# Performance work log

Measured on AMD Instinct MI355X. Metric: run time of the kernel, lower is better.

The kernel has to match this reference:

```python
import jax, jax.numpy as jnp
import numpy as np

ODE_UNFOLDS = 6
MOTOR_SIZE = 3
EPS = 1e-8

def _conv(x, w, b, stride):
    y = jax.lax.conv_general_dilated(x, w, (stride, stride), 'VALID',
                                     dimension_numbers=('NCHW', 'OIHW', 'NCHW'))
    return jax.nn.relu(y + b[None, :, None, None])

def _conv_head(x, w1, b1, w2, b2, w3, b3, w4, b4, w5, b5, fc_w, fc_b):
    # x: [B, T, 3, 66, 200] -> features [B, T, 128]
    B, T = x.shape[0], x.shape[1]
    h = x.reshape(B * T, *x.shape[2:])
    h = _conv(h, w1, b1, 2)  # [BT,24,31,98]
    h = _conv(h, w2, b2, 2)  # [BT,36,14,47]
    h = _conv(h, w3, b3, 2)  # [BT,48,5,22]
    h = _conv(h, w4, b4, 1)  # [BT,64,3,20]
    h = _conv(h, w5, b5, 1)  # [BT,64,1,18]
    h = h.reshape(B * T, -1)
    h = jax.nn.relu(h @ fc_w + fc_b)
    return h.reshape(B, T, -1)

def _ltc_step(inputs, v, s_mu, s_sigma, s_w, s_erev, mu, sigma, w, erev, gleak, vleak, cm):
    # inputs: [B,S], v: [B,N]
    # sensory synapse activations (constant over the ODE unfolds)
    s_act = s_w * jax.nn.sigmoid((inputs[:, :, None] - s_mu) * s_sigma)  # [B,S,N]
    w_num_s = jnp.sum(s_act * s_erev, axis=1)  # [B,N]
    w_den_s = jnp.sum(s_act, axis=1)           # [B,N]
    cm_t = cm * ODE_UNFOLDS  # cm / (elapsed=1 / ode_unfolds)
    for _ in range(ODE_UNFOLDS):
        w_act = w * jax.nn.sigmoid((v[:, :, None] - mu) * sigma)  # [B,N,N]
        w_num = jnp.sum(w_act * erev, axis=1) + w_num_s
        w_den = jnp.sum(w_act, axis=1) + w_den_s
        v = (cm_t * v + gleak * vleak + w_num) / (cm_t + gleak + w_den + EPS)
    return v[:, :MOTOR_SIZE], v

def reference(x, w1, b1, w2, b2, w3, b3, w4, b4, w5, b5, fc_w, fc_b,
              s_mu, s_sigma, s_w, s_erev, mu, sigma, w, erev, gleak, vleak, cm):
    y = _conv_head(x, w1, b1, w2, b2, w3, b3, w4, b4, w5, b5, fc_w, fc_b)  # [B,T,128]
    B, T, _ = y.shape
    N = mu.shape[0]
    v0 = jnp.zeros((B, N), dtype=y.dtype)

    def step(v, inp):
        out, v = _ltc_step(inp, v, s_mu, s_sigma, s_w, s_erev, mu, sigma, w, erev, gleak, vleak, cm)
        return v, out

    _, outs = jax.lax.scan(step, v0, jnp.swapaxes(y, 0, 1))  # outs: [T,B,3]
    return jnp.swapaxes(outs, 0, 1)  # [B,T,3]

def setup_inputs() -> dict:
    key = jax.random.key(0)
    ks = jax.random.split(key, 24)
    d = {}
    d['x'] = jax.random.normal(ks[0], (32, 16, 3, 66, 200), jnp.float32)
    shapes = [((24, 3, 5, 5), (24,)), ((36, 24, 5, 5), (36,)), ((48, 36, 5, 5), (48,)),
              ((64, 48, 3, 3), (64,)), ((64, 64, 3, 3), (64,))]
    for i, (ws, bs) in enumerate(shapes):
        d[f'w{i+1}'] = jax.random.normal(ks[1 + i], ws, jnp.float32) * 0.05
        d[f'b{i+1}'] = jnp.zeros(bs, jnp.float32)
    d['fc_w'] = jax.random.normal(ks[6], (1152, 128), jnp.float32) * 0.05
    d['fc_b'] = jnp.zeros((128,), jnp.float32)
    S, N = 128, 64
    d['s_mu'] = jax.random.normal(ks[7], (S, N), jnp.float32) * 0.3 + 0.3
    d['s_sigma'] = jax.random.uniform(ks[8], (S, N), jnp.float32, 3.0, 8.0)
    d['s_w'] = jax.random.uniform(ks[9], (S, N), jnp.float32, 0.001, 1.0)
    d['s_erev'] = jnp.sign(jax.random.normal(ks[10], (S, N), jnp.float32))
    d['mu'] = jax.random.normal(ks[11], (N, N), jnp.float32) * 0.3 + 0.3
    d['sigma'] = jax.random.uniform(ks[12], (N, N), jnp.float32, 3.0, 8.0)
    d['w'] = jax.random.uniform(ks[13], (N, N), jnp.float32, 0.001, 1.0)
    d['erev'] = jnp.sign(jax.random.normal(ks[14], (N, N), jnp.float32))
    d['gleak'] = jax.random.uniform(ks[15], (N,), jnp.float32, 0.001, 1.0)
    d['vleak'] = jax.random.uniform(ks[16], (N,), jnp.float32, -0.2, 0.2)
    d['cm'] = jax.random.uniform(ks[17], (N,), jnp.float32, 0.4, 0.6)
    return d
```

## Files before the change

### kernel.cpp

```cpp
#include <hip/hip_runtime.h>
#include <hip/hip_bf16.h>


typedef _Float16 f16;
typedef _Float16 f16x8 __attribute__((ext_vector_type(8)));
typedef _Float16 f16x4 __attribute__((ext_vector_type(4)));
typedef float    f32x4 __attribute__((ext_vector_type(4)));
typedef unsigned int u32;

static __device__ __forceinline__ float sigmoidf_fast(float x) {
    return __builtin_amdgcn_rcpf(1.0f + __expf(-x));
}


__global__ __launch_bounds__(256)
void wpack1_kernel(const float* __restrict__ w1, f16* __restrict__ Wpk1)
{
    int idx = blockIdx.x * 256 + threadIdx.x;
    if (idx >= 32 * 136) return;
    int co = idx / 136;
    int kk = idx % 136;
    float v = 0.0f;
    if (co < 24 && kk < 120) {
        int p = kk >> 3, jj = kk & 7;
        int kh = p / 3, kwp = p % 3;
        int kws = jj >> 2, ci = jj & 3;
        int kw = 2 * kwp + kws;
        if (kw < 5 && ci < 3)
            v = w1[(((size_t)co * 3 + ci) * 5 + kh) * 5 + kw];
    }
    Wpk1[idx] = (f16)v;
}

__global__ __launch_bounds__(512)
void conv1_mfma(const float* __restrict__ x, const f16* __restrict__ Wpk1,
                const float* __restrict__ b1, f16* __restrict__ h1T)
{
    __shared__ __align__(16) f16 img[52800];
    __shared__ __align__(16) f16 Wl[4352];

    int m    = blockIdx.x;
    int tid  = threadIdx.x;
    int lane = tid & 63;
    int wv   = tid >> 6;
    int col  = lane & 15;
    int row4 = lane >> 4;

    for (int u = tid; u < 544; u += 512)
        *(uint4*)((char*)Wl + (size_t)u * 16) =
            *(const uint4*)((const char*)Wpk1 + (size_t)u * 16);

    const float* xb = x + (size_t)m * 39600;
    for (int u = tid; u < 13200; u += 512) {
        float a = xb[u], b = xb[13200 + u], c = xb[26400 + u];
        f16x4 pk = { (f16)a, (f16)b, (f16)c, (f16)0.0f };
        *(f16x4*)(&img[(size_t)u * 4]) = pk;
    }
    __syncthreads();

    f16x8 af[2][4];
    #pragma unroll
    for (int Mt = 0; Mt < 2; ++Mt)
        #pragma unroll
        for (int t = 0; t < 4; ++t)
            af[Mt][t] = *(const f16x8*)((const char*)Wl +
                           (Mt * 16 + col) * 272 + t * 64 + row4 * 16);

    int rowB[4], kwpv[4];
    #pragma unroll
    for (int t = 0; t < 4; ++t) {
        int p = 4 * t + row4; if (p > 14) p = 14;
        rowB[t] = (p / 3) * 1600;
        kwpv[t] = (p % 3) * 16;
    }

    float bvv[2][4];
    #pragma unroll
    for (int Mt = 0; Mt < 2; ++Mt)
        #pragma unroll
        for (int i = 0; i < 4; ++i) {
            int co = Mt * 16 + row4 * 4 + i;
            bvv[Mt][i] = (co < 24) ? b1[co] : 0.0f;
        }

    const char* ic = (const char*)img;
    for (int it = 0; it < 24; ++it) {
        int s = wv + it * 8;
        if (s * 16 >= 3038) continue;
        int px = s * 16 + col;
        bool pv = (px < 3038);
        int pc = pv ? px : 3037;
        int ho = pc / 98;
        int wo = pc - ho * 98;
        int base = ho * 3200 + wo * 16;

        f32x4 a0 = {0.f,0.f,0.f,0.f}, a1 = {0.f,0.f,0.f,0.f};
        #pragma unroll
        for (int t = 0; t < 4; ++t) {
            f16x8 xf = *(const f16x8*)(ic + base + rowB[t] + kwpv[t]);
            a0 = __builtin_amdgcn_mfma_f32_16x16x32_f16(af[0][t], xf, a0, 0, 0, 0);
            a1 = __builtin_amdgcn_mfma_f32_16x16x32_f16(af[1][t], xf, a1, 0, 0, 0);
        }

        if (pv) {
            int key = (wo >> 1) & 7;
            size_t rowbase = ((size_t)m * 31 + ho) * 296;
            int j0 = (row4 & 1) * 4;
            {
                int c8 = row4 >> 1;
                f16x4 pk = { (f16)fmaxf(a0[0] + bvv[0][0], 0.0f),
                             (f16)fmaxf(a0[1] + bvv[0][1], 0.0f),
                             (f16)fmaxf(a0[2] + bvv[0][2], 0.0f),
                             (f16)fmaxf(a0[3] + bvv[0][3], 0.0f) };
                int sl = (3 * wo + c8) ^ key;
                *(f16x4*)(h1T + (rowbase + sl) * 8 + j0) = pk;
            }
            if (row4 < 2) {
                f16x4 pk = { (f16)fmaxf(a1[0] + bvv[1][0], 0.0f),
                             (f16)fmaxf(a1[1] + bvv[1][1], 0.0f),
                             (f16)fmaxf(a1[2] + bvv[1][2], 0.0f),
                             (f16)fmaxf(a1[3] + bvv[1][3], 0.0f) };
                int sl = (3 * wo + 2) ^ key;
                *(f16x4*)(h1T + (rowbase + sl) * 8 + j0) = pk;
            }
        }
    }
}

__global__ __launch_bounds__(256)
void wpack_kernel(const float* __restrict__ w2, f16* __restrict__ Wpk)
{
    int idx = blockIdx.x * 256 + threadIdx.x;
    if (idx >= 48 * 616) return;
    int co = idx / 616;
    int kk = idx % 616;
    float v = 0.0f;
    if (kk < 608 && co < 36) {
        int c = kk >> 3, j = kk & 7;
        if (c < 75) {
            int pq = c / 3, c8 = c - 3 * pq;
            int kh = pq / 5, kw = pq - 5 * kh;
            int ci = c8 * 8 + j;
            v = w2[(((size_t)co * 24 + ci) * 5 + kh) * 5 + kw];
        }
    }
    Wpk[idx] = (f16)v;
}

__global__ __launch_bounds__(256)
void wpack3_kernel(const float* __restrict__ w3, f16* __restrict__ Wpk3)
{
    int idx = blockIdx.x * 256 + threadIdx.x;
    if (idx >= 48 * 1032) return;
    int co = idx / 1032;
    int kk = idx % 1032;
    float v = 0.0f;
    if (kk < 1024) {
        int c = kk >> 3, j = kk & 7;
        int pq = c / 5, c8 = c - 5 * pq;
        if (pq < 25) {
            int kh = pq / 5, kw = pq - 5 * kh;
            int ci = c8 * 8 + j;
            if (ci < 36)
                v = w3[(((size_t)co * 36 + ci) * 5 + kh) * 5 + kw];
        }
    }
    Wpk3[idx] = (f16)v;
}

__global__ __launch_bounds__(384)
void conv2_mfma(const f16* __restrict__ h1T, const f16* __restrict__ Wpk,
                const float* __restrict__ b2, f16* __restrict__ h2f)
{
    __shared__ __align__(16) f16 Wl[48 * 616];
    __shared__ __align__(16) f16 tl[2][7 * 2368];
    __shared__ u32 lutS[76];

    int m    = blockIdx.x;
    int tid  = threadIdx.x;
    int lane = tid & 63;
    int wv   = tid >> 6;
    int ct   = wv >> 1;
    int sh   = wv & 1;
    int row4 = lane >> 4;
    int col  = lane & 15;

    if (tid < 76) {
        int c = tid; u32 v = 0;
        if (c < 75) {
            int pq = c / 3, c8 = c - 3 * pq;
            int kh = pq / 5, kw = pq - 5 * kh;
            v = ((u32)(kh * 4736) << 8) | ((u32)(kw >> 1) << 4) | (u32)(3 * kw + c8);
        }
        lutS[c] = v;
    }

    for (int u = tid; u < 3696; u += 384) {
        uint4 v = *(const uint4*)((const char*)Wpk + (size_t)u * 16);
        *(uint4*)((char*)Wl + (size_t)u * 16) = v;
    }

    int six_wo[3], wokey[3], rpoff[3], valid[3];
    #pragma unroll
    for (int si = 0; si < 3; ++si) {
        int s  = 3 * sh + si;
        int px = 16 * s + col;
        int rp = (px >= 48) ? 1 : 0;
        int wo = px - 48 * rp;
        valid[si] = (wo < 47);
        int wog = wo < 47 ? wo : 46;
        six_wo[si] = 6 * wog;
        wokey[si]  = wog;
        rpoff[si]  = rp * 9472;
    }
    int Abase = (ct * 16 + col) * 1232 + row4 * 16;
    float bv[4];
    #pragma unroll
    for (int i = 0; i < 4; ++i) {
        int co = ct * 16 + row4 * 4 + i;
        bv[i] = (co < 36) ? b2[co] : 0.0f;
    }
    int c8o = ct * 2 + (row4 >> 1);
    int hsel = (row4 & 1) * 4;

    uint4 stg[6];
    const f16* imgbase = h1T + (size_t)m * 31 * 2368;

    {
        const char* g = (const char*)(imgbase);
        #pragma unroll
        for (int i = 0; i < 6; ++i) {
            int u = tid + i * 384;
            if (u < 2072) *(uint4*)((char*)tl[0] + (size_t)u * 16) =
                              *(const uint4*)(g + (size_t)u * 16);
        }
    }
    __syncthreads();

    const char* Wc = (const char*)Wl;
    for (int p = 0; p < 7; ++p) {
        int cur = p & 1;
        if (p < 6) {
            const char* g = (const char*)(imgbase + (size_t)(4 * (p + 1)) * 2368);
            #pragma unroll
            for (int i = 0; i < 6; ++i) {
                int u = tid + i * 384;
                if (u < 2072) stg[i] = *(const uint4*)(g + (size_t)u * 16);
            }
        }

        const char* tb = (const char*)tl[cur];
        f32x4 acc0 = {0.f,0.f,0.f,0.f}, acc1 = {0.f,0.f,0.f,0.f}, acc2 = {0.f,0.f,0.f,0.f};
        #pragma unroll
        for (int t = 0; t < 19; ++t) {
            u32 lv   = lutS[4 * t + row4];
            int rowb = (int)(lv >> 8);
            int kwh  = (int)((lv >> 4) & 3);
            int ofs3 = (int)(lv & 15);
            f16x8 af = *(const f16x8*)(Wc + Abase + 64 * t);
            {
                int u0 = six_wo[0] + ofs3, k0 = (wokey[0] + kwh) & 7;
                f16x8 xf = *(const f16x8*)(tb + rpoff[0] + rowb + ((u0 ^ k0) << 4));
                acc0 = __builtin_amdgcn_mfma_f32_16x16x32_f16(af, xf, acc0, 0, 0, 0);
            }
            {
                int u1 = six_wo[1] + ofs3, k1 = (wokey[1] + kwh) & 7;
                f16x8 xf = *(const f16x8*)(tb + rpoff[1] + rowb + ((u1 ^ k1) << 4));
                acc1 = __builtin_amdgcn_mfma_f32_16x16x32_f16(af, xf, acc1, 0, 0, 0);
            }
            {
                int u2 = six_wo[2] + ofs3, k2 = (wokey[2] + kwh) & 7;
                f16x8 xf = *(const f16x8*)(tb + rpoff[2] + rowb + ((u2 ^ k2) << 4));
                acc2 = __builtin_amdgcn_mfma_f32_16x16x32_f16(af, xf, acc2, 0, 0, 0);
            }
        }

        #pragma unroll
        for (int si = 0; si < 3; ++si) {
            f32x4 a = (si == 0) ? acc0 : (si == 1) ? acc1 : acc2;
            int s  = 3 * sh + si;
            int px = 16 * s + col;
            int rp = (px >= 48) ? 1 : 0;
            int wo = px - 48 * rp;
            int ho = 2 * p + rp;
            if (valid[si] && c8o < 5) {
                f16x4 pk;
                #pragma unroll
                for (int i = 0; i < 4; ++i) pk[i] = (f16)fmaxf(a[i] + bv[i], 0.0f);
                int sl = (5 * wo + c8o) ^ ((wo >> 1) & 7);
                *(f16x4*)(h2f + ((size_t)m * 3374 + (size_t)ho * 241 + sl) * 8 + hsel) = pk;
            }
        }

        if (p < 6) {
            #pragma unroll
            for (int i = 0; i < 6; ++i) {
                int u = tid + i * 384;
                if (u < 2072) *(uint4*)((char*)tl[cur ^ 1] + (size_t)u * 16) = stg[i];
            }
        }
        __syncthreads();
    }
}

__global__ __launch_bounds__(384)
void conv3_mfma(const f16* __restrict__ h2f, const f16* __restrict__ Wpk3,
                const float* __restrict__ b3, float* __restrict__ h3)
{
    __shared__ __align__(16) f16 Wl[48 * 1032];
    __shared__ __align__(16) f16 img[3374 * 8];
    __shared__ u32 lut[128];

    int m    = blockIdx.x;
    int tid  = threadIdx.x;
    int lane = tid & 63;
    int wv   = tid >> 6;
    int ct   = wv >> 1;
    int sh   = wv & 1;
    int row4 = lane >> 4;
    int col  = lane & 15;

    if (tid < 128) {
        int c  = tid;
        int pq = c / 5, c8 = c - 5 * pq;
        int kh = pq / 5, kw = pq - 5 * kh;
        lut[c] = ((u32)(kh * 3856) << 8) | ((u32)(kw >> 1) << 5) | (u32)(5 * kw + c8);
    }
    for (int u = tid; u < 6192; u += 384)
        *(uint4*)((char*)Wl + (size_t)u * 16) =
            *(const uint4*)((const char*)Wpk3 + (size_t)u * 16);
    {
        const char* g = (const char*)(h2f + (size_t)m * 3374 * 8);
        for (int u = tid; u < 3374; u += 384)
            *(uint4*)((char*)img + (size_t)u * 16) = *(const uint4*)(g + (size_t)u * 16);
    }
    __syncthreads();

    int rb[4], wo10[4], wkey[4], valid[4], hov[4], wov[4];
    int nsi = 4 - sh;
    #pragma unroll
    for (int si = 0; si < 4; ++si) {
        int s  = 4 * sh + si;
        int px = 16 * s + col;
        valid[si] = (si < nsi) && (px < 110);
        int pc = px < 110 ? px : 109;
        int ho = pc / 22, wo = pc - 22 * ho;
        rb[si]   = ho * 7712;
        wo10[si] = 10 * wo;
        wkey[si] = wo;
        hov[si]  = ho; wov[si] = wo;
    }

    float bv[4];
    #pragma unroll
    for (int i = 0; i < 4; ++i) bv[i] = b3[ct * 16 + row4 * 4 + i];

    int Abase = (ct * 16 + col) * 2064 + row4 * 16;
    const char* Wc = (const char*)Wl;
    const char* ic = (const char*)img;

    f32x4 a0 = {0.f,0.f,0.f,0.f}, a1 = {0.f,0.f,0.f,0.f};
    f32x4 a2 = {0.f,0.f,0.f,0.f}, a3 = {0.f,0.f,0.f,0.f};
    #pragma unroll 8
    for (int t = 0; t < 32; ++t) {
        u32 lv     = lut[4 * t + row4];
        int rowoff = (int)(lv >> 8);
        int kwh    = (int)((lv >> 5) & 7);
        int b5     = (int)(lv & 31);
        f16x8 af = *(const f16x8*)(Wc + Abase + 64 * t);
        {
            int u = wo10[0] + b5, k = (wkey[0] + kwh) & 7;
            f16x8 xf = *(const f16x8*)(ic + rb[0] + rowoff + ((u ^ k) << 4));
            a0 = __builtin_amdgcn_mfma_f32_16x16x32_f16(af, xf, a0, 0, 0, 0);
        }
        {
            int u = wo10[1] + b5, k = (wkey[1] + kwh) & 7;
            f16x8 xf = *(const f16x8*)(ic + rb[1] + rowoff + ((u ^ k) << 4));
            a1 = __builtin_amdgcn_mfma_f32_16x16x32_f16(af, xf, a1, 0, 0, 0);
        }
        {
            int u = wo10[2] + b5, k = (wkey[2] + kwh) & 7;
            f16x8 xf = *(const f16x8*)(ic + rb[2] + rowoff + ((u ^ k) << 4));
            a2 = __builtin_amdgcn_mfma_f32_16x16x32_f16(af, xf, a2, 0, 0, 0);
        }
        {
            int u = wo10[3] + b5, k = (wkey[3] + kwh) & 7;
            f16x8 xf = *(const f16x8*)(ic + rb[3] + rowoff + ((u ^ k) << 4));
            a3 = __builtin_amdgcn_mfma_f32_16x16x32_f16(af, xf, a3, 0, 0, 0);
        }
    }

    int co0 = ct * 16 + row4 * 4;
    #pragma unroll
    for (int si = 0; si < 4; ++si) {
        if (!valid[si]) continue;
        f32x4 a = (si == 0) ? a0 : (si == 1) ? a1 : (si == 2) ? a2 : a3;
        float* op = h3 + (((size_t)m * 48 + co0) * 5 + hov[si]) * 22 + wov[si];
        #pragma unroll
        for (int i = 0; i < 4; ++i)
            op[(size_t)i * 110] = fmaxf(a[i] + bv[i], 0.0f);
    }
}

template<int CIN, int KH, int KW, int STRIDE, int CO_T, int WO_T>
__global__ __launch_bounds__(256)
void conv_tile_kernel(const float* __restrict__ in, const float* __restrict__ wt,
                      const float* __restrict__ bias, float* __restrict__ out,
                      int Cout, int Hin, int Win, int Hout, int Wout,
                      int n_cg, int n_wg, int M)
{
    constexpr int LOAD_W = (WO_T - 1) * STRIDE + KW;

    int bx = blockIdx.x;
    int cg = bx % n_cg;
    int gid = (bx / n_cg) * blockDim.x + threadIdx.x;
    int wg = gid % n_wg;
    int t  = gid / n_wg;
    int ho = t % Hout;
    int m  = t / Hout;
    if (m >= M) return;

    int wo0 = wg * WO_T;
    int co0 = cg * CO_T;

    const float* ip = in + ((size_t)(m * CIN) * Hin + (size_t)ho * STRIDE) * Win
                         + (size_t)wo0 * STRIDE;
    const float* wp = wt + (size_t)co0 * (CIN * KH * KW);

    float acc[CO_T][WO_T];
    #pragma unroll
    for (int c = 0; c < CO_T; ++c) {
        float b = bias[co0 + c];
        #pragma unroll
        for (int q = 0; q < WO_T; ++q) acc[c][q] = b;
    }

    #pragma unroll 1
    for (int ci = 0; ci < CIN; ++ci) {
        #pragma unroll
        for (int kh = 0; kh < KH; ++kh) {
            const float* row = ip + ((size_t)ci * Hin + kh) * Win;
            float xv[LOAD_W];
            #pragma unroll
            for (int l = 0; l < LOAD_W; ++l) xv[l] = row[l];
            const float* wrow = wp + (ci * KH + kh) * KW;
            #pragma unroll
            for (int c = 0; c < CO_T; ++c) {
                #pragma unroll
                for (int kw = 0; kw < KW; ++kw) {
                    float wv = wrow[c * (CIN * KH * KW) + kw];
                    #pragma unroll
                    for (int q = 0; q < WO_T; ++q)
                        acc[c][q] = fmaf(xv[q * STRIDE + kw], wv, acc[c][q]);
                }
            }
        }
    }

    #pragma unroll
    for (int c = 0; c < CO_T; ++c) {
        float* op = out + (((size_t)m * Cout + co0 + c) * Hout + ho) * Wout + wo0;
        #pragma unroll
        for (int q = 0; q < WO_T; ++q) {
            if (wo0 + q < Wout) op[q] = fmaxf(acc[c][q], 0.0f);
        }
    }
}

__global__ __launch_bounds__(256)
void fc_relu_kernel(const float* __restrict__ h, const float* __restrict__ w,
                    const float* __restrict__ b, float* __restrict__ out)
{
    __shared__ float hs[1152];
    __shared__ float part[8][32][4];
    int f   = blockIdx.x;
    int tid = threadIdx.x;
    int ks  = tid >> 5;
    int j4  = tid & 31;
    for (int k = tid; k < 1152; k += 256) hs[k] = h[(size_t)f * 1152 + k];
    __syncthreads();
    const float4* w4 = (const float4*)w;
    float4 acc = {0.f, 0.f, 0.f, 0.f};
    int k0 = ks * 144;
    #pragma unroll 4
    for (int kk = 0; kk < 144; ++kk) {
        int k = k0 + kk;
        float4 wv = w4[(size_t)k * 32 + j4];
        float hb = hs[k];
        acc.x = fmaf(wv.x, hb, acc.x);
        acc.y = fmaf(wv.y, hb, acc.y);
        acc.z = fmaf(wv.z, hb, acc.z);
        acc.w = fmaf(wv.w, hb, acc.w);
    }
    *(float4*)&part[ks][j4][0] = acc;
    __syncthreads();
    if (tid < 128) {
        int j = tid, jq = j >> 2, r = j & 3;
        float s = b[j];
        #pragma unroll
        for (int q = 0; q < 8; ++q) s += part[q][jq][r];
        out[(size_t)f * 128 + j] = fmaxf(s, 0.0f);
    }
}

__global__ __launch_bounds__(64)
void sensory_kernel(const float* __restrict__ feat,
                    const float* __restrict__ s_mu,
                    const float* __restrict__ s_sigma,
                    const float* __restrict__ s_w,
                    const float* __restrict__ s_erev,
                    float* __restrict__ wnum, float* __restrict__ wden)
{
    __shared__ float y[128];
    int bt = blockIdx.x;
    int n  = threadIdx.x;
    for (int s = n; s < 128; s += 64) y[s] = feat[bt * 128 + s];
    __syncthreads();
    float num = 0.0f, den = 0.0f;
    for (int s = 0; s < 128; ++s) {
        int o = s * 64 + n;
        float a = s_w[o] * sigmoidf_fast((y[s] - s_mu[o]) * s_sigma[o]);
        num = fmaf(a, s_erev[o], num);
        den += a;
    }
    wnum[bt * 64 + n] = num;
    wden[bt * 64 + n] = den;
}

__global__ __launch_bounds__(512)
void ltc_wave_kernel(const float* __restrict__ wnum_s,
                     const float* __restrict__ wden_s,
                     const float* __restrict__ mu, const float* __restrict__ sigma,
                     const float* __restrict__ w, const float* __restrict__ erev,
                     const float* __restrict__ gleak, const float* __restrict__ vleak,
                     const float* __restrict__ cm, float* __restrict__ out, int T)
{
    __shared__ float2 pnd[2][8][64];

    int b    = blockIdx.x;
    int tid  = threadIdx.x;
    int lane = tid & 63;
    int p    = tid >> 6;

    float musig[8], nsg[8], wv[8], wev[8];
    #pragma unroll
    for (int ii = 0; ii < 8; ++ii) {
        int o = (8 * p + ii) * 64 + lane;
        float sg = sigma[o];
        musig[ii] = mu[o] * sg;
        nsg[ii]   = -sg;
        float wl  = w[o];
        wv[ii]    = wl;
        wev[ii]   = wl * erev[o];
    }
    float gl   = gleak[lane];
    float glvl = gl * vleak[lane];
    float cmt  = cm[lane] * 6.0f;
    float v    = 0.0f;
    int   buf  = 0;

    for (int t = 0; t < T; ++t) {
        float ns = wnum_s[(b * T + t) * 64 + lane];
        float ds = wden_s[(b * T + t) * 64 + lane];
        #pragma unroll 1
        for (int u = 0; u < 6; ++u) {
            float num = 0.0f, den = 0.0f;
            #pragma unroll
            for (int ii = 0; ii < 8; ++ii) {
                float vi  = __shfl(v, 8 * p + ii);
                float arg = fmaf(vi, nsg[ii], musig[ii]);
                float e   = __expf(arg);
                float s   = __builtin_amdgcn_rcpf(1.0f + e);
                den = fmaf(wv[ii], s, den);
                num = fmaf(wev[ii], s, num);
            }
            pnd[buf][p][lane] = make_float2(num, den);
            __syncthreads();
            float wn = ns, wd = ds;
            #pragma unroll
            for (int q = 0; q < 8; ++q) {
                float2 pq = pnd[buf][q][lane];
                wn += pq.x; wd += pq.y;
            }
            v = (fmaf(cmt, v, glvl) + wn) *
                __builtin_amdgcn_rcpf(cmt + gl + wd + 1e-8f);
            buf ^= 1;
        }
        if (tid < 3) out[(b * T + t) * 3 + tid] = v;
    }
}

extern "C" void kernel_launch(void* const* d_in, const int* in_sizes, int n_in,
                              void* d_out, int out_size, void* d_ws, size_t ws_size,
                              hipStream_t stream)
{
    (void)in_sizes; (void)n_in; (void)out_size; (void)ws_size;

    const float* x    = (const float*)d_in[0];
    const float* w1   = (const float*)d_in[1];
    const float* b1   = (const float*)d_in[2];
    const float* w2   = (const float*)d_in[3];
    const float* b2   = (const float*)d_in[4];
    const float* w3   = (const float*)d_in[5];
    const float* b3   = (const float*)d_in[6];
    const float* w4   = (const float*)d_in[7];
    const float* b4   = (const float*)d_in[8];
    const float* w5   = (const float*)d_in[9];
    const float* b5   = (const float*)d_in[10];
    const float* fcw  = (const float*)d_in[11];
    const float* fcb  = (const float*)d_in[12];
    const float* smu  = (const float*)d_in[13];
    const float* ssig = (const float*)d_in[14];
    const float* sw   = (const float*)d_in[15];
    const float* serv = (const float*)d_in[16];
    const float* mu   = (const float*)d_in[17];
    const float* sig  = (const float*)d_in[18];
    const float* ww   = (const float*)d_in[19];
    const float* erev = (const float*)d_in[20];
    const float* gl   = (const float*)d_in[21];
    const float* vl   = (const float*)d_in[22];
    const float* cm   = (const float*)d_in[23];
    float* out = (float*)d_out;

    const int BT = 512;

    char* wsB = (char*)d_ws;
    size_t off = 0;
    f16*   h1T  = (f16*)(wsB + off); off += (size_t)512 * 31 * 2368 * 2;
    f16*   Wpk  = (f16*)(wsB + off); off += 65536;
    f16*   h2f  = (f16*)(wsB + off); off += (size_t)512 * 3374 * 16;
    f16*   Wpk3 = (f16*)(wsB + off); off += 48 * 1032 * 2;
    f16*   Wpk1 = (f16*)(wsB + off); off += 32 * 136 * 2;
    float* h3   = (float*)(wsB + off); off += (size_t)512 * 48 * 5 * 22 * 4;
    float* h4   = (float*)(wsB + off); off += (size_t)512 * 64 * 3 * 20 * 4;
    float* h5   = (float*)(wsB + off); off += (size_t)512 * 64 * 18 * 4;
    float* feat = (float*)(wsB + off); off += (size_t)BT * 128 * 4;
    float* wnum = (float*)(wsB + off); off += (size_t)BT * 64 * 4;
    float* wden = (float*)(wsB + off); off += (size_t)BT * 64 * 4;

    wpack1_kernel<<<(32 * 136 + 255) / 256, 256, 0, stream>>>(w1, Wpk1);
    wpack_kernel<<<(48 * 616 + 255) / 256, 256, 0, stream>>>(w2, Wpk);
    wpack3_kernel<<<(48 * 1032 + 255) / 256, 256, 0, stream>>>(w3, Wpk3);

    conv1_mfma<<<512, 512, 0, stream>>>(x, Wpk1, b1, h1T);
    conv2_mfma<<<512, 384, 0, stream>>>(h1T, Wpk, b2, h2f);
    conv3_mfma<<<512, 384, 0, stream>>>(h2f, Wpk3, b3, h3);

    {
        int n_cg = 16, n_wg = 5;
        int sp_threads = BT * 3 * n_wg;
        int grid = (sp_threads + 255) / 256 * n_cg;
        conv_tile_kernel<48, 3, 3, 1, 4, 4><<<grid, 256, 0, stream>>>(
            h3, w4, b4, h4, 64, 5, 22, 3, 20, n_cg, n_wg, BT);
    }
    {
        int n_cg = 16, n_wg = 6;
        int sp_threads = BT * 1 * n_wg;
        int grid = (sp_threads + 255) / 256 * n_cg;
        conv_tile_kernel<64, 3, 3, 1, 4, 3><<<grid, 256, 0, stream>>>(
            h4, w5, b5, h5, 64, 3, 20, 1, 18, n_cg, n_wg, BT);
    }
    fc_relu_kernel<<<512, 256, 0, stream>>>(h5, fcw, fcb, feat);
    sensory_kernel<<<BT, 64, 0, stream>>>(feat, smu, ssig, sw, serv, wnum, wden);
    ltc_wave_kernel<<<32, 512, 0, stream>>>(wnum, wden, mu, sig, ww, erev,
                                            gl, vl, cm, out, 16);
}
```

Baseline: 296.8 us.

## Use parity-split channel-major layouts for conv1/conv2 outputs and keep conv2 weights in registers

Replaces the XOR-swizzled interleaved layout of intermediate activations with a channel-group-major, even/odd-column-split layout. Strided convolution reads become contiguous per lane, and the address math drops to a single add of a LUT offset. conv2 also stops staging weights in LDS and holds its 19 A-fragments in registers, which frees shared memory so the kernel can declare three blocks per CU. The trade-off is higher register pressure, and the new layout may introduce LDS bank conflicts that the swizzle used to avoid.

```diff
diff --git a/kernel.cpp b/kernel.cpp
--- a/kernel.cpp
+++ b/kernel.cpp
@@ -103,8 +103,8 @@
         }
 
         if (pv) {
-            int key = (wo >> 1) & 7;
             size_t rowbase = ((size_t)m * 31 + ho) * 296;
+            int par = (wo & 1) * 49, wh = wo >> 1;
             int j0 = (row4 & 1) * 4;
             {
                 int c8 = row4 >> 1;
@@ -112,7 +112,7 @@
                              (f16)fmaxf(a0[1] + bvv[0][1], 0.0f),
                              (f16)fmaxf(a0[2] + bvv[0][2], 0.0f),
                              (f16)fmaxf(a0[3] + bvv[0][3], 0.0f) };
-                int sl = (3 * wo + c8) ^ key;
+                int sl = c8 * 98 + par + wh;
                 *(f16x4*)(h1T + (rowbase + sl) * 8 + j0) = pk;
             }
             if (row4 < 2) {
@@ -120,7 +120,7 @@
                              (f16)fmaxf(a1[1] + bvv[1][1], 0.0f),
                              (f16)fmaxf(a1[2] + bvv[1][2], 0.0f),
                              (f16)fmaxf(a1[3] + bvv[1][3], 0.0f) };
-                int sl = (3 * wo + 2) ^ key;
+                int sl = 2 * 98 + par + wh;
                 *(f16x4*)(h1T + (rowbase + sl) * 8 + j0) = pk;
             }
         }
@@ -168,11 +168,10 @@
     Wpk3[idx] = (f16)v;
 }
 
-__global__ __launch_bounds__(384)
+__global__ __launch_bounds__(384, 3)
 void conv2_mfma(const f16* __restrict__ h1T, const f16* __restrict__ Wpk,
                 const float* __restrict__ b2, f16* __restrict__ h2f)
 {
-    __shared__ __align__(16) f16 Wl[48 * 616];
     __shared__ __align__(16) f16 tl[2][7 * 2368];
     __shared__ u32 lutS[76];
 
@@ -190,17 +189,21 @@
         if (c < 75) {
             int pq = c / 3, c8 = c - 3 * pq;
             int kh = pq / 5, kw = pq - 5 * kh;
-            v = ((u32)(kh * 4736) << 8) | ((u32)(kw >> 1) << 4) | (u32)(3 * kw + c8);
+            u32 ofs = (u32)(c8 * 98 + (kw & 1) * 49 + (kw >> 1));
+            v = ((u32)(kh * 4736) << 8) | ofs;
         }
         lutS[c] = v;
     }
 
-    for (int u = tid; u < 3696; u += 384) {
-        uint4 v = *(const uint4*)((const char*)Wpk + (size_t)u * 16);
-        *(uint4*)((char*)Wl + (size_t)u * 16) = v;
-    }
-
-    int six_wo[3], wokey[3], rpoff[3], valid[3];
+    f16x8 af[19];
+    {
+        const char* wb = (const char*)Wpk + (size_t)(ct * 16 + col) * 1232 + row4 * 16;
+        #pragma unroll
+        for (int t = 0; t < 19; ++t)
+            af[t] = *(const f16x8*)(wb + t * 64);
+    }
+
+    int wo16[3], rpoff[3], valid[3], wov[3];
     #pragma unroll
     for (int si = 0; si < 3; ++si) {
         int s  = 3 * sh + si;
@@ -209,18 +212,17 @@
         int wo = px - 48 * rp;
         valid[si] = (wo < 47);
         int wog = wo < 47 ? wo : 46;
-        six_wo[si] = 6 * wog;
-        wokey[si]  = wog;
-        rpoff[si]  = rp * 9472;
-    }
-    int Abase = (ct * 16 + col) * 1232 + row4 * 16;
+        wo16[si]  = wog * 16;
+        wov[si]   = wo;
+        rpoff[si] = rp * 9472;
+    }
     float bv[4];
     #pragma unroll
     for (int i = 0; i < 4; ++i) {
         int co = ct * 16 + row4 * 4 + i;
         bv[i] = (co < 36) ? b2[co] : 0.0f;
     }
-    int c8o = ct * 2 + (row4 >> 1);
+    int c8o  = ct * 2 + (row4 >> 1);
     int hsel = (row4 & 1) * 4;
 
     uint4 stg[6];
@@ -237,7 +239,6 @@
     }
     __syncthreads();
 
-    const char* Wc = (const char*)Wl;
     for (int p = 0; p < 7; ++p) {
         int cur = p & 1;
         if (p < 6) {
@@ -255,23 +256,19 @@
         for (int t = 0; t < 19; ++t) {
             u32 lv   = lutS[4 * t + row4];
             int rowb = (int)(lv >> 8);
-            int kwh  = (int)((lv >> 4) & 3);
-            int ofs3 = (int)(lv & 15);
-            f16x8 af = *(const f16x8*)(Wc + Abase + 64 * t);
+            int boff = (int)(lv & 255) << 4;
+            f16x8 a = af[t];
             {
-                int u0 = six_wo[0] + ofs3, k0 = (wokey[0] + kwh) & 7;
-                f16x8 xf = *(const f16x8*)(tb + rpoff[0] + rowb + ((u0 ^ k0) << 4));
-                acc0 = __builtin_amdgcn_mfma_f32_16x16x32_f16(af, xf, acc0, 0, 0, 0);
+                f16x8 xf = *(const f16x8*)(tb + rpoff[0] + rowb + boff + wo16[0]);
+                acc0 = __builtin_amdgcn_mfma_f32_16x16x32_f16(a, xf, acc0, 0, 0, 0);
             }
             {
-                int u1 = six_wo[1] + ofs3, k1 = (wokey[1] + kwh) & 7;
-                f16x8 xf = *(const f16x8*)(tb + rpoff[1] + rowb + ((u1 ^ k1) << 4));
-                acc1 = __builtin_amdgcn_mfma_f32_16x16x32_f16(af, xf, acc1, 0, 0, 0);
+                f16x8 xf = *(const f16x8*)(tb + rpoff[1] + rowb + boff + wo16[1]);
+                acc1 = __builtin_amdgcn_mfma_f32_16x16x32_f16(a, xf, acc1, 0, 0, 0);
             }
             {
-                int u2 = six_wo[2] + ofs3, k2 = (wokey[2] + kwh) & 7;
-                f16x8 xf = *(const f16x8*)(tb + rpoff[2] + rowb + ((u2 ^ k2) << 4));
-                acc2 = __builtin_amdgcn_mfma_f32_16x16x32_f16(af, xf, acc2, 0, 0, 0);
+                f16x8 xf = *(const f16x8*)(tb + rpoff[2] + rowb + boff + wo16[2]);
+                acc2 = __builtin_amdgcn_mfma_f32_16x16x32_f16(a, xf, acc2, 0, 0, 0);
             }
         }
 
@@ -287,7 +284,7 @@
                 f16x4 pk;
                 #pragma unroll
                 for (int i = 0; i < 4; ++i) pk[i] = (f16)fmaxf(a[i] + bv[i], 0.0f);
-                int sl = (5 * wo + c8o) ^ ((wo >> 1) & 7);
+                int sl = c8o * 47 + (wo & 1) * 24 + (wo >> 1);
                 *(f16x4*)(h2f + ((size_t)m * 3374 + (size_t)ho * 241 + sl) * 8 + hsel) = pk;
             }
         }
@@ -324,7 +321,8 @@
         int c  = tid;
         int pq = c / 5, c8 = c - 5 * pq;
         int kh = pq / 5, kw = pq - 5 * kh;
-        lut[c] = ((u32)(kh * 3856) << 8) | ((u32)(kw >> 1) << 5) | (u32)(5 * kw + c8);
+        lut[c] = ((u32)(kh * 3856) << 8) |
+                 (u32)(c8 * 47 + (kw & 1) * 24 + (kw >> 1));
     }
     for (int u = tid; u < 6192; u += 384)
         *(uint4*)((char*)Wl + (size_t)u * 16) =
@@ -336,7 +334,7 @@
     }
     __syncthreads();
 
-    int rb[4], wo10[4], wkey[4], valid[4], hov[4], wov[4];
+    int rb[4], wo16[4], valid[4], hov[4], wov[4];
     int nsi = 4 - sh;
     #pragma unroll
     for (int si = 0; si < 4; ++si) {
@@ -346,8 +344,7 @@
         int pc = px < 110 ? px : 109;
         int ho = pc / 22, wo = pc - 22 * ho;
         rb[si]   = ho * 7712;
-        wo10[si] = 10 * wo;
-        wkey[si] = wo;
+        wo16[si] = wo * 16;
         hov[si]  = ho; wov[si] = wo;
     }
 
@@ -365,27 +362,22 @@
     for (int t = 0; t < 32; ++t) {
         u32 lv     = lut[4 * t + row4];
         int rowoff = (int)(lv >> 8);
-        int kwh    = (int)((lv >> 5) & 7);
-        int b5     = (int)(lv & 31);
+        int boff   = (int)(lv & 255) << 4;
         f16x8 af = *(const f16x8*)(Wc + Abase + 64 * t);
         {
-            int u = wo10[0] + b5, k = (wkey[0] + kwh) & 7;
-            f16x8 xf = *(const f16x8*)(ic + rb[0] + rowoff + ((u ^ k) << 4));
+            f16x8 xf = *(const f16x8*)(ic + rb[0] + rowoff + boff + wo16[0]);
             a0 = __builtin_amdgcn_mfma_f32_16x16x32_f16(af, xf, a0, 0, 0, 0);
         }
         {
-            int u = wo10[1] + b5, k = (wkey[1] + kwh) & 7;
-            f16x8 xf = *(const f16x8*)(ic + rb[1] + rowoff + ((u ^ k) << 4));
+            f16x8 xf = *(const f16x8*)(ic + rb[1] + rowoff + boff + wo16[1]);
             a1 = __builtin_amdgcn_mfma_f32_16x16x32_f16(af, xf, a1, 0, 0, 0);
         }
         {
-            int u = wo10[2] + b5, k = (wkey[2] + kwh) & 7;
-            f16x8 xf = *(const f16x8*)(ic + rb[2] + rowoff + ((u ^ k) << 4));
+            f16x8 xf = *(const f16x8*)(ic + rb[2] + rowoff + boff + wo16[2]);
             a2 = __builtin_amdgcn_mfma_f32_16x16x32_f16(af, xf, a2, 0, 0, 0);
         }
         {
-            int u = wo10[3] + b5, k = (wkey[3] + kwh) & 7;
-            f16x8 xf = *(const f16x8*)(ic + rb[3] + rowoff + ((u ^ k) << 4));
+            f16x8 xf = *(const f16x8*)(ic + rb[3] + rowoff + boff + wo16[3]);
             a3 = __builtin_amdgcn_mfma_f32_16x16x32_f16(af, xf, a3, 0, 0, 0);
         }
     }
```

After: 286.8 us. -3.4%, faster.
